# Kernel optimization log

Hardware: AMD Instinct MI355X
Metric: run time of the kernel (lower is better)

Reference implementation:

```python
import jax, jax.numpy as jnp
import numpy as np


def setup_inputs() -> dict:
    key = jax.random.key(0)
    kx, kq, kv = jax.random.split(key, 3)
    B, S, D = 4, 2048, 64
    # positive inputs + nonnegative W_Q guarantee diagonal scores > threshold t=1,
    # so no softmax column is fully -inf (the original would NaN on symmetric data).
    x = jax.random.uniform(kx, (B, S, D), dtype=jnp.float32)
    std = 1.0 / np.sqrt(S)  # xavier_normal for an SxS matrix: sqrt(2/(S+S))
    W_Q = jnp.abs(jax.random.normal(kq, (S, S), dtype=jnp.float32) * std)
    W_V = jax.random.normal(kv, (S, S), dtype=jnp.float32) * std
    return {"x": x, "W_Q": W_Q, "W_V": W_V}


def reference(x, W_Q, W_V):
    B, S, D = x.shape
    t = 1.0  # sigma threshold
    neg_inf = jnp.asarray(-jnp.inf, x.dtype)

    # V = W_V @ T  (contract over the token axis)
    V = jnp.einsum('st,btd->bsd', W_V, x)

    # G = running mean of tokens (cumsum / position). Original divides by
    # arange(0, S) which is a divide-by-zero bug at position 0; we use the
    # intended running-mean denominator 1..S.
    denom = jnp.arange(1, S + 1, dtype=x.dtype)[None, :, None]  # [1,S,1]
    G = jnp.cumsum(x, axis=1) / denom

    Q = jnp.einsum('st,btd->bsd', W_Q, G)          # [B,S,D]
    scores = jnp.einsum('bid,bjd->bij', Q, x)      # Q @ K^T, K = x

    # sigma: values <= t -> -inf
    scores = jnp.where(scores <= t, neg_inf, scores)

    # causal mask M: -inf strictly above the diagonal
    causal = jnp.triu(jnp.full((S, S), neg_inf, dtype=x.dtype), k=1)
    A = scores + causal

    # NOTE: original softmax is over dim=1 (the query axis), kept faithfully.
    P = jax.nn.softmax(A / jnp.sqrt(jnp.asarray(S, x.dtype)), axis=1)
    return jnp.einsum('bij,bjd->bid', P, V)
```

## Files before the change

### kernel.cpp

```cpp
#include <hip/hip_runtime.h>

typedef unsigned short u16;
typedef __bf16 bf16;
typedef bf16 bf16x8 __attribute__((ext_vector_type(8)));
typedef float f32x4 __attribute__((ext_vector_type(4)));

#define S 2048
#define D 64
#define BATCH 4
#define SCL 0.022097086912079612f

__device__ __forceinline__ u16 f2bf(float f) {
  union { float f; unsigned u; } v; v.f = f;
  return (u16)((v.u + 0x7FFFu + ((v.u >> 16) & 1u)) >> 16);
}

__device__ __forceinline__ void gld16(const u16* g, u16* l) {
  __builtin_amdgcn_global_load_lds(
      (const __attribute__((address_space(1))) unsigned int*)(const void*)g,
      (__attribute__((address_space(3))) unsigned int*)(void*)l, 16, 0, 0);
}

__global__ void k_pre(const float* __restrict__ x,
                      const float* __restrict__ wq, const float* __restrict__ wv,
                      u16* __restrict__ wqp, u16* __restrict__ wvb,
                      u16* __restrict__ xb, u16* __restrict__ xTb) {
  int bx = blockIdx.x, t = threadIdx.x;
  if (bx < 512) {
    int m = bx * 4 + (t >> 6);
    int l = t & 63;
    const float* row = wq + (size_t)m * S;
    u16* orow = wqp + (size_t)m * S;
    float4 f[8];
#pragma unroll
    for (int c = 0; c < 8; ++c) f[c] = *(const float4*)(row + c * 256 + l * 4);
#pragma unroll
    for (int c = 0; c < 8; ++c) {
      int base = c * 256 + l * 4;
      f[c].x /= (float)(base + 1); f[c].y /= (float)(base + 2);
      f[c].z /= (float)(base + 3); f[c].w /= (float)(base + 4);
    }
    float carry = 0.f;
#pragma unroll
    for (int c = 7; c >= 0; --c) {
      float4 v = f[c];
      float sl = v.x + v.y + v.z + v.w;
      float s = sl;
#pragma unroll
      for (int off = 1; off < 64; off <<= 1) {
        float o = __shfl_down(s, off);
        s += (l + off < 64) ? o : 0.f;
      }
      float tot = __shfl(s, 0);
      float excl = s - sl;
      float s3 = v.w, s2 = v.z + s3, s1 = v.y + s2, s0 = v.x + s1;
      union { u16 q[4]; ushort4 u4; } o;
      o.q[0] = f2bf(carry + excl + s0);
      o.q[1] = f2bf(carry + excl + s1);
      o.q[2] = f2bf(carry + excl + s2);
      o.q[3] = f2bf(carry + excl + s3);
      *(ushort4*)(orow + c * 256 + l * 4) = o.u4;
      carry += tot;
    }
  } else if (bx < 1536) {
    size_t idx = ((size_t)(bx - 512) * 256 + t) * 16;
#pragma unroll
    for (int h = 0; h < 2; ++h) {
      const float* src = wv + idx + h * 8;
      float4 a = *(const float4*)src;
      float4 b = *(const float4*)(src + 4);
      union { u16 s[8]; uint4 v; } u;
      u.s[0]=f2bf(a.x); u.s[1]=f2bf(a.y); u.s[2]=f2bf(a.z); u.s[3]=f2bf(a.w);
      u.s[4]=f2bf(b.x); u.s[5]=f2bf(b.y); u.s[6]=f2bf(b.z); u.s[7]=f2bf(b.w);
      *(uint4*)(wvb + idx + h * 8) = u.v;
    }
  } else {
    int job = (bx - 1536) * 4 + (t >> 6);
    int chunk = job >> 2, b = job & 3, d = t & 63;
    const float* xp = x + ((size_t)b * S + (size_t)chunk * 16) * D + d;
#pragma unroll
    for (int s = 0; s < 16; ++s) {
      float v = xp[(size_t)s * D];
      int sg = chunk * 16 + s;
      u16 h = f2bf(v);
      xb[((size_t)b * S + sg) * D + d] = h;
      xTb[((size_t)b * D + d) * S + sg] = h;
    }
  }
}

__global__ __launch_bounds__(128) void k_wg(
    const u16* __restrict__ wqp, const u16* __restrict__ wvb,
    const u16* __restrict__ xTb,
    u16* __restrict__ Qb, u16* __restrict__ VTb) {
  __shared__ u16 Ab[2][32 * 128];
  __shared__ u16 Bb[2][32 * 128];
  int bx = blockIdx.x;
  int nt = bx >> 7, mg = bx & 127;
  int mat = mg >> 6;
  int mrow = (mg & 63) * 32;
  int t = threadIdx.x;
  int w = t >> 6, l = t & 63;
  int lr = l & 15, lg = l >> 4;
  const u16* A = (mat ? wvb : wqp) + (size_t)mrow * S;
  const u16* BT = xTb + (size_t)(nt * 32) * S;
  int rA = t >> 4;
  int sb = t & 15;
  int swz = ((sb & 8) | ((sb & 7) ^ (rA & 7))) * 8;
  const u16* Ag = A + (size_t)rA * S + swz;
  const u16* Bg = BT + (size_t)rA * S + swz;
  f32x4 acc[2] = {};

  auto stage = [&](int buf, int kt) {
#pragma unroll
    for (int i = 0; i < 4; ++i)
      gld16(Ag + kt * 128 + (size_t)i * 8 * S, &Ab[buf][i * 1024 + t * 8]);
#pragma unroll
    for (int i = 0; i < 4; ++i)
      gld16(Bg + kt * 128 + (size_t)i * 8 * S, &Bb[buf][i * 1024 + t * 8]);
  };

  stage(0, 0);
  __syncthreads();
  int buf = 0;
  for (int kt = 0; kt < 16; ++kt) {
    if (kt < 15) stage(buf ^ 1, kt + 1);
    bf16x8 af[4], bfv[2][4];
#pragma unroll
    for (int ks = 0; ks < 4; ++ks) {
      int row = w * 16 + lr;
      int s = ks * 4 + lg;
      int col = ((s & 8) | ((s & 7) ^ (lr & 7))) * 8;
      af[ks] = *(const bf16x8*)&Ab[buf][row * 128 + col];
    }
#pragma unroll
    for (int nf = 0; nf < 2; ++nf)
#pragma unroll
      for (int ks = 0; ks < 4; ++ks) {
        int row = nf * 16 + lr;
        int s = ks * 4 + lg;
        int col = ((s & 8) | ((s & 7) ^ (lr & 7))) * 8;
        bfv[nf][ks] = *(const bf16x8*)&Bb[buf][row * 128 + col];
      }
#pragma unroll
    for (int ks = 0; ks < 4; ++ks)
#pragma unroll
      for (int nf = 0; nf < 2; ++nf)
        acc[nf] = __builtin_amdgcn_mfma_f32_16x16x32_bf16(af[ks], bfv[nf][ks], acc[nf], 0, 0, 0);
    __syncthreads();
    buf ^= 1;
  }
  int mbase = mrow + w * 16 + lg * 4;
#pragma unroll
  for (int nf = 0; nf < 2; ++nf) {
    int n = nt * 32 + nf * 16 + lr;
    int b = n >> 6, d = n & 63;
    if (mat == 0) {
#pragma unroll
      for (int r = 0; r < 4; ++r)
        Qb[((size_t)b * S + mbase + r) * D + d] = f2bf(acc[nf][r]);
    } else {
      union { u16 s[4]; ushort4 v; } u;
#pragma unroll
      for (int r = 0; r < 4; ++r) u.s[r] = f2bf(acc[nf][r]);
      *(ushort4*)&VTb[((size_t)b * D + d) * S + mbase] = u.v;
    }
  }
}

__global__ __launch_bounds__(256) void k_stats(
    const u16* __restrict__ xb, const u16* __restrict__ Qb,
    float* __restrict__ rzbuf, float* __restrict__ out) {
  __shared__ float zs[4][16];
  int jg = blockIdx.x, b = blockIdx.y;
  int tid = threadIdx.x;
  {
    size_t zi = ((size_t)(b * 128 + jg) * 256 + tid) * 4;
    *(float4*)(out + zi) = make_float4(0.f, 0.f, 0.f, 0.f);
  }
  int w = tid >> 6, l = tid & 63;
  int lr = l & 15, lg = l >> 4;
  int j0 = jg * 16;
  const u16* xbase = xb + (size_t)b * S * D;
  const u16* qbase = Qb + (size_t)b * S * D;
  bf16x8 xa0 = *(const bf16x8*)(xbase + (size_t)(j0 + lr) * D + lg * 8);
  bf16x8 xa1 = *(const bf16x8*)(xbase + (size_t)(j0 + lr) * D + 32 + lg * 8);
  float z[4] = {0.f, 0.f, 0.f, 0.f};
  for (int i16 = j0 + w * 16; i16 < S; i16 += 128) {
    {
      bf16x8 q0 = *(const bf16x8*)(qbase + (size_t)(i16 + lr) * D + lg * 8);
      bf16x8 q1 = *(const bf16x8*)(qbase + (size_t)(i16 + lr) * D + 32 + lg * 8);
      f32x4 c = {};
      c = __builtin_amdgcn_mfma_f32_16x16x32_bf16(xa0, q0, c, 0, 0, 0);
      c = __builtin_amdgcn_mfma_f32_16x16x32_bf16(xa1, q1, c, 0, 0, 0);
      int i = i16 + lr;
#pragma unroll
      for (int r = 0; r < 4; ++r) {
        int j = j0 + lg * 4 + r;
        float sc = c[r];
        z[r] += (i >= j && sc > 1.0f) ? __expf(sc * SCL) : 0.f;
      }
    }
    int i16b = i16 + 64;
    if (i16b < S) {
      bf16x8 q0 = *(const bf16x8*)(qbase + (size_t)(i16b + lr) * D + lg * 8);
      bf16x8 q1 = *(const bf16x8*)(qbase + (size_t)(i16b + lr) * D + 32 + lg * 8);
      f32x4 c = {};
      c = __builtin_amdgcn_mfma_f32_16x16x32_bf16(xa0, q0, c, 0, 0, 0);
      c = __builtin_amdgcn_mfma_f32_16x16x32_bf16(xa1, q1, c, 0, 0, 0);
      int i = i16b + lr;
#pragma unroll
      for (int r = 0; r < 4; ++r) {
        int j = j0 + lg * 4 + r;
        float sc = c[r];
        z[r] += (i >= j && sc > 1.0f) ? __expf(sc * SCL) : 0.f;
      }
    }
  }
#pragma unroll
  for (int r = 0; r < 4; ++r) {
    z[r] += __shfl_xor(z[r], 1);
    z[r] += __shfl_xor(z[r], 2);
    z[r] += __shfl_xor(z[r], 4);
    z[r] += __shfl_xor(z[r], 8);
  }
  if (lr == 0) {
#pragma unroll
    for (int r = 0; r < 4; ++r) zs[w][lg * 4 + r] = z[r];
  }
  __syncthreads();
  if (tid < 16) {
    float zf = zs[0][tid] + zs[1][tid] + zs[2][tid] + zs[3][tid];
    rzbuf[(size_t)b * S + j0 + tid] = 1.0f / zf;
  }
}

__global__ __launch_bounds__(256) void k_out(
    const u16* __restrict__ xb, const u16* __restrict__ Qb, const u16* __restrict__ VTb,
    const float* __restrict__ rzbuf, float* __restrict__ out) {
  __shared__ u16 Plds[4][16][72];
  int bx = 143 - blockIdx.x, b = blockIdx.y;
  int it = 0, jc = 0, base = 0;
  for (int tt = 0; tt < 32; ++tt) {
    int nc = (tt + 4) >> 2;
    if (bx < base + nc) { it = tt; jc = bx - base; break; }
    base += nc;
  }
  int w = threadIdx.x >> 6, l = threadIdx.x & 63;
  int lr = l & 15, lg = l >> 4;
  int i0 = it * 64 + w * 16;
  const u16* xbase = xb + (size_t)b * S * D;
  const u16* qbase = Qb + (size_t)b * S * D;
  const u16* vbase = VTb + (size_t)b * D * S;
  const float* rzb = rzbuf + (size_t)b * S;
  bf16x8 qa0 = *(const bf16x8*)(qbase + (size_t)(i0 + lr) * D + lg * 8);
  bf16x8 qa1 = *(const bf16x8*)(qbase + (size_t)(i0 + lr) * D + 32 + lg * 8);
  f32x4 acc[4] = {};
  int jt_end = min(jc * 4 + 4, it + 1);
  for (int jt = jc * 4; jt < jt_end; ++jt) {
#pragma unroll
    for (int js = 0; js < 4; ++js) {
      int j16 = jt * 64 + js * 16;
      bf16x8 xb0 = *(const bf16x8*)(xbase + (size_t)(j16 + lr) * D + lg * 8);
      bf16x8 xb1 = *(const bf16x8*)(xbase + (size_t)(j16 + lr) * D + 32 + lg * 8);
      f32x4 c = {};
      c = __builtin_amdgcn_mfma_f32_16x16x32_bf16(qa0, xb0, c, 0, 0, 0);
      c = __builtin_amdgcn_mfma_f32_16x16x32_bf16(qa1, xb1, c, 0, 0, 0);
      int j = j16 + lr;
      float rzj = rzb[j];
#pragma unroll
      for (int r = 0; r < 4; ++r) {
        int i = i0 + lg * 4 + r;
        float sc = c[r];
        float wgt = (j <= i && sc > 1.0f) ? __expf(sc * SCL) * rzj : 0.f;
        Plds[w][lg * 4 + r][js * 16 + lr] = f2bf(wgt);
      }
    }
    asm volatile("s_waitcnt lgkmcnt(0)" ::: "memory");
    __builtin_amdgcn_s_setprio(1);
#pragma unroll
    for (int kk = 0; kk < 2; ++kk) {
      bf16x8 pa = *(const bf16x8*)(&Plds[w][lr][kk * 32 + lg * 8]);
#pragma unroll
      for (int dt = 0; dt < 4; ++dt) {
        bf16x8 vbf = *(const bf16x8*)(vbase + (size_t)(dt * 16 + lr) * S + jt * 64 + kk * 32 + lg * 8);
        acc[dt] = __builtin_amdgcn_mfma_f32_16x16x32_bf16(pa, vbf, acc[dt], 0, 0, 0);
      }
    }
    __builtin_amdgcn_s_setprio(0);
    asm volatile("s_waitcnt lgkmcnt(0)" ::: "memory");
  }
  float* obase = out + (size_t)b * S * D;
#pragma unroll
  for (int dt = 0; dt < 4; ++dt)
#pragma unroll
    for (int r = 0; r < 4; ++r) {
      int i = i0 + lg * 4 + r;
      atomicAdd(&obase[(size_t)i * D + dt * 16 + lr], acc[dt][r]);
    }
}

extern "C" void kernel_launch(void* const* d_in, const int* in_sizes, int n_in,
                              void* d_out, int out_size, void* d_ws, size_t ws_size,
                              hipStream_t stream) {
  const float* x  = (const float*)d_in[0];
  const float* wq = (const float*)d_in[1];
  const float* wv = (const float*)d_in[2];
  float* out = (float*)d_out;
  char* ws = (char*)d_ws;
  size_t off = 0;
  auto alloc = [&](size_t bytes) -> void* {
    void* p = ws + off; off += (bytes + 255) & ~255ULL; return p;
  };
  u16* xb   = (u16*)alloc((size_t)BATCH * S * D * 2);
  u16* xTb  = (u16*)alloc((size_t)BATCH * S * D * 2);
  u16* Qb   = (u16*)alloc((size_t)BATCH * S * D * 2);
  u16* VTb  = (u16*)alloc((size_t)BATCH * S * D * 2);
  float* rzbuf = (float*)alloc((size_t)BATCH * S * 4);
  u16* wqp  = (u16*)alloc((size_t)S * S * 2);
  u16* wvb  = (u16*)alloc((size_t)S * S * 2);

  k_pre<<<1664, 256, 0, stream>>>(x, wq, wv, wqp, wvb, xb, xTb);
  k_wg<<<1024, 128, 0, stream>>>(wqp, wvb, xTb, Qb, VTb);
  k_stats<<<dim3(128, BATCH), 256, 0, stream>>>(xb, Qb, rzbuf, out);
  k_out<<<dim3(144, BATCH), 256, 0, stream>>>(xb, Qb, VTb, rzbuf, out);
}
```

Before: 72.39 us.

## Materialize exp-scores matrix in stats pass and fold normalization into V

The stats kernel now writes each masked, exponentiated score as bf16 into a full B×S×S buffer while it accumulates column sums. It then scales the V^T columns by the reciprocal sums. The output kernel no longer recomputes QK^T and exp; it streams the stored E rows directly as MFMA operands against the pre-scaled V, with finer 2-tile work chunks and more blocks. This removes the duplicated score computation and the LDS staging. In exchange it adds roughly 32MB of scattered column-strided 2-byte global writes and a matching large read, so memory traffic is the new bottleneck risk.

```diff
diff --git a/kernel.cpp b/kernel.cpp
--- a/kernel.cpp
+++ b/kernel.cpp
@@ -13,6 +13,10 @@
 __device__ __forceinline__ u16 f2bf(float f) {
   union { float f; unsigned u; } v; v.f = f;
   return (u16)((v.u + 0x7FFFu + ((v.u >> 16) & 1u)) >> 16);
+}
+
+__device__ __forceinline__ float bf2f(u16 h) {
+  union { unsigned u; float f; } v; v.u = ((unsigned)h) << 16; return v.f;
 }
 
 __device__ __forceinline__ void gld16(const u16* g, u16* l) {
@@ -170,8 +174,9 @@
 
 __global__ __launch_bounds__(256) void k_stats(
     const u16* __restrict__ xb, const u16* __restrict__ Qb,
-    float* __restrict__ rzbuf, float* __restrict__ out) {
+    u16* __restrict__ Eb, u16* __restrict__ VTb, float* __restrict__ out) {
   __shared__ float zs[4][16];
+  __shared__ float rzs[16];
   int jg = blockIdx.x, b = blockIdx.y;
   int tid = threadIdx.x;
   {
@@ -183,112 +188,80 @@
   int j0 = jg * 16;
   const u16* xbase = xb + (size_t)b * S * D;
   const u16* qbase = Qb + (size_t)b * S * D;
+  u16* ebase = Eb + (size_t)b * S * S;
+  int rbase = j0 & ~63;
+  for (int e = tid; e < (j0 - rbase) * 16; e += 256)
+    ebase[(size_t)(rbase + (e >> 4)) * S + j0 + (e & 15)] = 0;
   bf16x8 xa0 = *(const bf16x8*)(xbase + (size_t)(j0 + lr) * D + lg * 8);
   bf16x8 xa1 = *(const bf16x8*)(xbase + (size_t)(j0 + lr) * D + 32 + lg * 8);
-  float z[4] = {0.f, 0.f, 0.f, 0.f};
-  for (int i16 = j0 + w * 16; i16 < S; i16 += 128) {
-    {
-      bf16x8 q0 = *(const bf16x8*)(qbase + (size_t)(i16 + lr) * D + lg * 8);
-      bf16x8 q1 = *(const bf16x8*)(qbase + (size_t)(i16 + lr) * D + 32 + lg * 8);
-      f32x4 c = {};
-      c = __builtin_amdgcn_mfma_f32_16x16x32_bf16(xa0, q0, c, 0, 0, 0);
-      c = __builtin_amdgcn_mfma_f32_16x16x32_bf16(xa1, q1, c, 0, 0, 0);
-      int i = i16 + lr;
-#pragma unroll
-      for (int r = 0; r < 4; ++r) {
-        int j = j0 + lg * 4 + r;
-        float sc = c[r];
-        z[r] += (i >= j && sc > 1.0f) ? __expf(sc * SCL) : 0.f;
-      }
-    }
-    int i16b = i16 + 64;
-    if (i16b < S) {
-      bf16x8 q0 = *(const bf16x8*)(qbase + (size_t)(i16b + lr) * D + lg * 8);
-      bf16x8 q1 = *(const bf16x8*)(qbase + (size_t)(i16b + lr) * D + 32 + lg * 8);
-      f32x4 c = {};
-      c = __builtin_amdgcn_mfma_f32_16x16x32_bf16(xa0, q0, c, 0, 0, 0);
-      c = __builtin_amdgcn_mfma_f32_16x16x32_bf16(xa1, q1, c, 0, 0, 0);
-      int i = i16b + lr;
-#pragma unroll
-      for (int r = 0; r < 4; ++r) {
-        int j = j0 + lg * 4 + r;
-        float sc = c[r];
-        z[r] += (i >= j && sc > 1.0f) ? __expf(sc * SCL) : 0.f;
-      }
-    }
-  }
-#pragma unroll
-  for (int r = 0; r < 4; ++r) {
-    z[r] += __shfl_xor(z[r], 1);
-    z[r] += __shfl_xor(z[r], 2);
-    z[r] += __shfl_xor(z[r], 4);
-    z[r] += __shfl_xor(z[r], 8);
-  }
-  if (lr == 0) {
-#pragma unroll
-    for (int r = 0; r < 4; ++r) zs[w][lg * 4 + r] = z[r];
-  }
+  int j = j0 + lr;
+  u16* ecol = ebase + j;
+  float zl = 0.f;
+  for (int i16 = j0 + w * 16; i16 < S; i16 += 64) {
+    bf16x8 q0 = *(const bf16x8*)(qbase + (size_t)(i16 + lr) * D + lg * 8);
+    bf16x8 q1 = *(const bf16x8*)(qbase + (size_t)(i16 + lr) * D + 32 + lg * 8);
+    f32x4 c = {};
+    c = __builtin_amdgcn_mfma_f32_16x16x32_bf16(q0, xa0, c, 0, 0, 0);
+    c = __builtin_amdgcn_mfma_f32_16x16x32_bf16(q1, xa1, c, 0, 0, 0);
+#pragma unroll
+    for (int r = 0; r < 4; ++r) {
+      int i = i16 + lg * 4 + r;
+      float sc = c[r];
+      float e = (i >= j && sc > 1.0f) ? __expf(sc * SCL) : 0.f;
+      zl += e;
+      ecol[(size_t)i * S] = f2bf(e);
+    }
+  }
+  zl += __shfl_xor(zl, 16);
+  zl += __shfl_xor(zl, 32);
+  if (l < 16) zs[w][l] = zl;
   __syncthreads();
   if (tid < 16) {
     float zf = zs[0][tid] + zs[1][tid] + zs[2][tid] + zs[3][tid];
-    rzbuf[(size_t)b * S + j0 + tid] = 1.0f / zf;
+    rzs[tid] = 1.0f / zf;
+  }
+  __syncthreads();
+  {
+    int d = tid & 63, jj = tid >> 6;
+    u16* vp = &VTb[((size_t)b * D + d) * S + j0 + jj * 4];
+    union { u16 s[4]; ushort4 v; } u;
+    u.v = *(ushort4*)vp;
+#pragma unroll
+    for (int k = 0; k < 4; ++k) u.s[k] = f2bf(bf2f(u.s[k]) * rzs[jj * 4 + k]);
+    *(ushort4*)vp = u.v;
   }
 }
 
 __global__ __launch_bounds__(256) void k_out(
-    const u16* __restrict__ xb, const u16* __restrict__ Qb, const u16* __restrict__ VTb,
-    const float* __restrict__ rzbuf, float* __restrict__ out) {
-  __shared__ u16 Plds[4][16][72];
-  int bx = 143 - blockIdx.x, b = blockIdx.y;
+    const u16* __restrict__ Eb, const u16* __restrict__ VTb,
+    float* __restrict__ out) {
+  int bx = 271 - blockIdx.x, b = blockIdx.y;
   int it = 0, jc = 0, base = 0;
   for (int tt = 0; tt < 32; ++tt) {
-    int nc = (tt + 4) >> 2;
+    int nc = (tt + 2) >> 1;
     if (bx < base + nc) { it = tt; jc = bx - base; break; }
     base += nc;
   }
   int w = threadIdx.x >> 6, l = threadIdx.x & 63;
   int lr = l & 15, lg = l >> 4;
   int i0 = it * 64 + w * 16;
-  const u16* xbase = xb + (size_t)b * S * D;
-  const u16* qbase = Qb + (size_t)b * S * D;
+  const u16* erow = Eb + (size_t)b * S * S + (size_t)(i0 + lr) * S;
   const u16* vbase = VTb + (size_t)b * D * S;
-  const float* rzb = rzbuf + (size_t)b * S;
-  bf16x8 qa0 = *(const bf16x8*)(qbase + (size_t)(i0 + lr) * D + lg * 8);
-  bf16x8 qa1 = *(const bf16x8*)(qbase + (size_t)(i0 + lr) * D + 32 + lg * 8);
   f32x4 acc[4] = {};
-  int jt_end = min(jc * 4 + 4, it + 1);
-  for (int jt = jc * 4; jt < jt_end; ++jt) {
-#pragma unroll
-    for (int js = 0; js < 4; ++js) {
-      int j16 = jt * 64 + js * 16;
-      bf16x8 xb0 = *(const bf16x8*)(xbase + (size_t)(j16 + lr) * D + lg * 8);
-      bf16x8 xb1 = *(const bf16x8*)(xbase + (size_t)(j16 + lr) * D + 32 + lg * 8);
-      f32x4 c = {};
-      c = __builtin_amdgcn_mfma_f32_16x16x32_bf16(qa0, xb0, c, 0, 0, 0);
-      c = __builtin_amdgcn_mfma_f32_16x16x32_bf16(qa1, xb1, c, 0, 0, 0);
-      int j = j16 + lr;
-      float rzj = rzb[j];
-#pragma unroll
-      for (int r = 0; r < 4; ++r) {
-        int i = i0 + lg * 4 + r;
-        float sc = c[r];
-        float wgt = (j <= i && sc > 1.0f) ? __expf(sc * SCL) * rzj : 0.f;
-        Plds[w][lg * 4 + r][js * 16 + lr] = f2bf(wgt);
-      }
-    }
-    asm volatile("s_waitcnt lgkmcnt(0)" ::: "memory");
-    __builtin_amdgcn_s_setprio(1);
+  int jt_end = min(jc * 2 + 2, it + 1);
+  for (int jt = jc * 2; jt < jt_end; ++jt) {
 #pragma unroll
     for (int kk = 0; kk < 2; ++kk) {
-      bf16x8 pa = *(const bf16x8*)(&Plds[w][lr][kk * 32 + lg * 8]);
+      int joff = jt * 64 + kk * 32 + lg * 8;
+      bf16x8 pa = *(const bf16x8*)(erow + joff);
+      __builtin_amdgcn_s_setprio(1);
 #pragma unroll
       for (int dt = 0; dt < 4; ++dt) {
-        bf16x8 vbf = *(const bf16x8*)(vbase + (size_t)(dt * 16 + lr) * S + jt * 64 + kk * 32 + lg * 8);
+        bf16x8 vbf = *(const bf16x8*)(vbase + (size_t)(dt * 16 + lr) * S + joff);
         acc[dt] = __builtin_amdgcn_mfma_f32_16x16x32_bf16(pa, vbf, acc[dt], 0, 0, 0);
       }
-    }
-    __builtin_amdgcn_s_setprio(0);
-    asm volatile("s_waitcnt lgkmcnt(0)" ::: "memory");
+      __builtin_amdgcn_s_setprio(0);
+    }
   }
   float* obase = out + (size_t)b * S * D;
 #pragma unroll
@@ -316,12 +289,12 @@
   u16* xTb  = (u16*)alloc((size_t)BATCH * S * D * 2);
   u16* Qb   = (u16*)alloc((size_t)BATCH * S * D * 2);
   u16* VTb  = (u16*)alloc((size_t)BATCH * S * D * 2);
-  float* rzbuf = (float*)alloc((size_t)BATCH * S * 4);
   u16* wqp  = (u16*)alloc((size_t)S * S * 2);
   u16* wvb  = (u16*)alloc((size_t)S * S * 2);
+  u16* Eb   = (u16*)alloc((size_t)BATCH * S * S * 2);
 
   k_pre<<<1664, 256, 0, stream>>>(x, wq, wv, wqp, wvb, xb, xTb);
   k_wg<<<1024, 128, 0, stream>>>(wqp, wvb, xTb, Qb, VTb);
-  k_stats<<<dim3(128, BATCH), 256, 0, stream>>>(xb, Qb, rzbuf, out);
-  k_out<<<dim3(144, BATCH), 256, 0, stream>>>(xb, Qb, VTb, rzbuf, out);
-}
+  k_stats<<<dim3(128, BATCH), 256, 0, stream>>>(xb, Qb, Eb, VTb, out);
+  k_out<<<dim3(272, BATCH), 256, 0, stream>>>(Eb, VTb, out);
+}
```

New measurement: 74.53 us. 1.03x slower.

## Fold softmax column normalizer into V and widen stats kernel to 512 threads

Applied to the files above, without the earlier changes.

The stats kernel now runs 8 waves per block, so each wave handles half as many query tiles. It then scales the bf16 transposed V rows by the per-column reciprocal normalizer directly, instead of writing a separate rz buffer. The output kernel no longer loads rz or multiplies by it in its inner loop. In exchange, V gets an extra bf16 round-trip, which adds rounding error, and the unnormalized exp weights stored as bf16 in P now have a larger dynamic range.

```diff
diff --git a/kernel.cpp b/kernel.cpp
--- a/kernel.cpp
+++ b/kernel.cpp
@@ -13,6 +13,10 @@
 __device__ __forceinline__ u16 f2bf(float f) {
   union { float f; unsigned u; } v; v.f = f;
   return (u16)((v.u + 0x7FFFu + ((v.u >> 16) & 1u)) >> 16);
+}
+
+__device__ __forceinline__ float bf2f(u16 h) {
+  union { unsigned u; float f; } v; v.u = ((unsigned)h) << 16; return v.f;
 }
 
 __device__ __forceinline__ void gld16(const u16* g, u16* l) {
@@ -168,13 +172,14 @@
   }
 }
 
-__global__ __launch_bounds__(256) void k_stats(
+__global__ __launch_bounds__(512) void k_stats(
     const u16* __restrict__ xb, const u16* __restrict__ Qb,
-    float* __restrict__ rzbuf, float* __restrict__ out) {
-  __shared__ float zs[4][16];
+    u16* __restrict__ VTb, float* __restrict__ out) {
+  __shared__ float zs[8][16];
+  __shared__ float rzs[16];
   int jg = blockIdx.x, b = blockIdx.y;
   int tid = threadIdx.x;
-  {
+  if (tid < 256) {
     size_t zi = ((size_t)(b * 128 + jg) * 256 + tid) * 4;
     *(float4*)(out + zi) = make_float4(0.f, 0.f, 0.f, 0.f);
   }
@@ -186,7 +191,7 @@
   bf16x8 xa0 = *(const bf16x8*)(xbase + (size_t)(j0 + lr) * D + lg * 8);
   bf16x8 xa1 = *(const bf16x8*)(xbase + (size_t)(j0 + lr) * D + 32 + lg * 8);
   float z[4] = {0.f, 0.f, 0.f, 0.f};
-  for (int i16 = j0 + w * 16; i16 < S; i16 += 128) {
+  for (int i16 = j0 + w * 16; i16 < S; i16 += 256) {
     {
       bf16x8 q0 = *(const bf16x8*)(qbase + (size_t)(i16 + lr) * D + lg * 8);
       bf16x8 q1 = *(const bf16x8*)(qbase + (size_t)(i16 + lr) * D + 32 + lg * 8);
@@ -201,7 +206,7 @@
         z[r] += (i >= j && sc > 1.0f) ? __expf(sc * SCL) : 0.f;
       }
     }
-    int i16b = i16 + 64;
+    int i16b = i16 + 128;
     if (i16b < S) {
       bf16x8 q0 = *(const bf16x8*)(qbase + (size_t)(i16b + lr) * D + lg * 8);
       bf16x8 q1 = *(const bf16x8*)(qbase + (size_t)(i16b + lr) * D + 32 + lg * 8);
@@ -230,14 +235,26 @@
   }
   __syncthreads();
   if (tid < 16) {
-    float zf = zs[0][tid] + zs[1][tid] + zs[2][tid] + zs[3][tid];
-    rzbuf[(size_t)b * S + j0 + tid] = 1.0f / zf;
+    float zf = 0.f;
+#pragma unroll
+    for (int ww = 0; ww < 8; ++ww) zf += zs[ww][tid];
+    rzs[tid] = 1.0f / zf;
+  }
+  __syncthreads();
+  if (tid < 256) {
+    int d = tid & 63, jj = tid >> 6;
+    u16* vp = &VTb[((size_t)b * D + d) * S + j0 + jj * 4];
+    union { u16 s[4]; ushort4 v; } u;
+    u.v = *(ushort4*)vp;
+#pragma unroll
+    for (int k = 0; k < 4; ++k) u.s[k] = f2bf(bf2f(u.s[k]) * rzs[jj * 4 + k]);
+    *(ushort4*)vp = u.v;
   }
 }
 
 __global__ __launch_bounds__(256) void k_out(
     const u16* __restrict__ xb, const u16* __restrict__ Qb, const u16* __restrict__ VTb,
-    const float* __restrict__ rzbuf, float* __restrict__ out) {
+    float* __restrict__ out) {
   __shared__ u16 Plds[4][16][72];
   int bx = 143 - blockIdx.x, b = blockIdx.y;
   int it = 0, jc = 0, base = 0;
@@ -252,7 +269,6 @@
   const u16* xbase = xb + (size_t)b * S * D;
   const u16* qbase = Qb + (size_t)b * S * D;
   const u16* vbase = VTb + (size_t)b * D * S;
-  const float* rzb = rzbuf + (size_t)b * S;
   bf16x8 qa0 = *(const bf16x8*)(qbase + (size_t)(i0 + lr) * D + lg * 8);
   bf16x8 qa1 = *(const bf16x8*)(qbase + (size_t)(i0 + lr) * D + 32 + lg * 8);
   f32x4 acc[4] = {};
@@ -267,12 +283,11 @@
       c = __builtin_amdgcn_mfma_f32_16x16x32_bf16(qa0, xb0, c, 0, 0, 0);
       c = __builtin_amdgcn_mfma_f32_16x16x32_bf16(qa1, xb1, c, 0, 0, 0);
       int j = j16 + lr;
-      float rzj = rzb[j];
 #pragma unroll
       for (int r = 0; r < 4; ++r) {
         int i = i0 + lg * 4 + r;
         float sc = c[r];
-        float wgt = (j <= i && sc > 1.0f) ? __expf(sc * SCL) * rzj : 0.f;
+        float wgt = (j <= i && sc > 1.0f) ? __expf(sc * SCL) : 0.f;
         Plds[w][lg * 4 + r][js * 16 + lr] = f2bf(wgt);
       }
     }
@@ -316,12 +331,11 @@
   u16* xTb  = (u16*)alloc((size_t)BATCH * S * D * 2);
   u16* Qb   = (u16*)alloc((size_t)BATCH * S * D * 2);
   u16* VTb  = (u16*)alloc((size_t)BATCH * S * D * 2);
-  float* rzbuf = (float*)alloc((size_t)BATCH * S * 4);
   u16* wqp  = (u16*)alloc((size_t)S * S * 2);
   u16* wvb  = (u16*)alloc((size_t)S * S * 2);
 
   k_pre<<<1664, 256, 0, stream>>>(x, wq, wv, wqp, wvb, xb, xTb);
   k_wg<<<1024, 128, 0, stream>>>(wqp, wvb, xTb, Qb, VTb);
-  k_stats<<<dim3(128, BATCH), 256, 0, stream>>>(xb, Qb, rzbuf, out);
-  k_out<<<dim3(144, BATCH), 256, 0, stream>>>(xb, Qb, VTb, rzbuf, out);
-}
+  k_stats<<<dim3(128, BATCH), 512, 0, stream>>>(xb, Qb, VTb, out);
+  k_out<<<dim3(144, BATCH), 256, 0, stream>>>(xb, Qb, VTb, out);
+}
```

New measurement: 73.07 us. About the same (+0.9%).
